# Performance work log

Measured on AMD Instinct MI355X. Metric: run time of the kernel, lower is better.

## Reference

```python
import jax, jax.numpy as jnp
import numpy as np

B, S, D, H = 2, 2048, 1024, 16
DEPTH = D // H


def setup_inputs() -> dict:
    key = jax.random.key(0)
    ks = jax.random.split(key, 10)
    std = 1.0 / np.sqrt(D)
    v = jax.random.normal(ks[0], (B, S, D), jnp.float32)
    q = jax.random.normal(ks[1], (B, S, D), jnp.float32)
    k = jax.random.normal(ks[2], (B, S, D), jnp.float32)
    # padding mask: 1.0 at masked (padded) key positions, 0.0 elsewhere
    mask = (jax.random.uniform(ks[3], (B, 1, 1, S)) < 0.1).astype(jnp.float32)
    Wq = jax.random.normal(ks[4], (D, D), jnp.float32) * std
    bq = jnp.zeros((D,), jnp.float32)
    Wv = jax.random.normal(ks[5], (D, D), jnp.float32) * std
    bv = jnp.zeros((D,), jnp.float32)
    Wo = jax.random.normal(ks[6], (D, D), jnp.float32) * std
    bo = jnp.zeros((D,), jnp.float32)
    return {"v": v, "q": q, "k": k, "mask": mask,
            "Wq": Wq, "bq": bq, "Wv": Wv, "bv": bv, "Wo": Wo, "bo": bo}


def _split_heads(x):
    # (B, S, D) -> (B, H, S, depth)
    return x.reshape(B, S, H, DEPTH).transpose(0, 2, 1, 3)


def reference(v, q, k, mask, Wq, bq, Wv, bv, Wo, bo):
    # NOTE: faithful to source, keys are projected with the QUERY weights
    # (mixedK = self.wQuery(k) in the original code).
    Q = _split_heads(q @ Wq + bq)
    K = _split_heads(k @ Wq + bq)
    V = _split_heads(v @ Wv + bv)
    scale = 1.0 / jnp.sqrt(jnp.asarray(DEPTH, jnp.float32))
    logits = jnp.einsum('bhqd,bhkd->bhqk', Q, K) * scale
    logits = logits + mask * (-1e9)
    attn = jax.nn.softmax(logits, axis=-1)
    out = jnp.einsum('bhqk,bhkd->bhqd', attn, V)
    out = out.transpose(0, 2, 1, 3).reshape(B, S, D)
    return out @ Wo + bo
```

## Files before the change

### kernel.cpp

```cpp
#include <hip/hip_runtime.h>
#include <cstddef>


namespace {

constexpr int Ss = 2048;
constexpr int Dd = 1024;
constexpr int Mm = 4096;
constexpr int NT = Ss / 64;
constexpr float QSCALE = 0.18033688f;
constexpr float NEG2 = -1.442695041e9f;

typedef unsigned short u16;
typedef __attribute__((ext_vector_type(8))) __bf16 bf16x8;
typedef __attribute__((ext_vector_type(4))) float f32x4;
typedef __attribute__((ext_vector_type(16))) float f32x16;
typedef __attribute__((ext_vector_type(4))) unsigned int u32x4;
typedef __attribute__((ext_vector_type(2))) unsigned int u32x2;

__device__ __forceinline__ u16 bfc(float f) {
  __bf16 h = (__bf16)f;
  return __builtin_bit_cast(u16, h);
}
__device__ __forceinline__ unsigned pack2(float lo, float hi) {
  return (unsigned)bfc(lo) | ((unsigned)bfc(hi) << 16);
}

__device__ __forceinline__ void gload_lds16(const void* g, void* l) {
  __builtin_amdgcn_global_load_lds(
      (__attribute__((address_space(1))) void*)g,
      (__attribute__((address_space(3))) void*)l, 16, 0, 0);
}

__device__ __forceinline__ f32x4 mfma16(bf16x8 a, bf16x8 b, f32x4 c) {
  return __builtin_amdgcn_mfma_f32_16x16x32_bf16(a, b, c, 0, 0, 0);
}
__device__ __forceinline__ f32x16 mfma32(bf16x8 a, bf16x8 b, f32x16 c) {
  return __builtin_amdgcn_mfma_f32_32x32x16_bf16(a, b, c, 0, 0, 0);
}
__device__ __forceinline__ float exp2_fast(float x) {
  return __builtin_amdgcn_exp2f(x);
}

__device__ __forceinline__ void pl32swap(unsigned& a, unsigned& b) {
#if __has_builtin(__builtin_amdgcn_permlane32_swap)
  u32x2 r = __builtin_amdgcn_permlane32_swap(a, b, false, false);
  a = r[0];
  b = r[1];
#else
  unsigned ax = (unsigned)__shfl_xor((int)a, 32);
  unsigned bx = (unsigned)__shfl_xor((int)b, 32);
  bool hi = (threadIdx.x & 63) >= 32;
  unsigned na = hi ? bx : a;
  unsigned nb = hi ? b : ax;
  a = na;
  b = nb;
#endif
}

__device__ __forceinline__ int swz(int row, int col) {
  return row * 64 + ((((col >> 3) ^ (row & 7)) << 3) | (col & 7));
}
__device__ __forceinline__ int src_col(int lane) {
  return ((lane & 7) ^ (lane >> 3)) * 8;
}

__global__ __launch_bounds__(256) void wt_transpose(const float* __restrict__ W0,
                                                    const float* __restrict__ W1,
                                                    const float* __restrict__ W2,
                                                    u16* __restrict__ wsbase) {
  const float* W = (blockIdx.z == 0) ? W0 : (blockIdx.z == 1) ? W1 : W2;
  u16* WT = wsbase + (size_t)blockIdx.z * (1024 * 1024);
  __shared__ float tile[32][33];
  const int tid = threadIdx.x;
  const int tx = tid & 31;
  const int ty = tid >> 5;
  const int n0 = blockIdx.x * 32;
  const int k0 = blockIdx.y * 32;
#pragma unroll
  for (int i = 0; i < 4; ++i)
    tile[ty + i * 8][tx] = W[(size_t)(k0 + ty + i * 8) * 1024 + n0 + tx];
  __syncthreads();
  const int r = tid >> 3;
  const int c4 = (tid & 7) * 4;
  ushort4 o4 = make_ushort4(bfc(tile[c4 + 0][r]), bfc(tile[c4 + 1][r]),
                            bfc(tile[c4 + 2][r]), bfc(tile[c4 + 3][r]));
  *(ushort4*)(&WT[(size_t)(n0 + r) * 1024 + k0 + c4]) = o4;
}

__global__ __launch_bounds__(256) void proj_qkv(
    const float* __restrict__ q, const float* __restrict__ k,
    const float* __restrict__ v, const u16* __restrict__ WqT,
    const u16* __restrict__ WvT, const float* __restrict__ bq,
    const float* __restrict__ bv, u16* __restrict__ Qp, u16* __restrict__ Kp,
    u16* __restrict__ VpT) {
  constexpr int K = 1024, N = 1024, M = 4096;
  __shared__ u16 As[128 * 64];
  __shared__ u16 Bs[128 * 64];
  const int lin = (int)blockIdx.x;
  const int xcd = lin & 7;
  const int j = lin >> 3;
  const int panel = xcd * 12 + (j >> 3);
  const int ntile = j & 7;
  const int z = panel >> 5;
  const int mtile = panel & 31;
  const int n0 = ntile * 128;
  const int m0 = mtile * 128;

  const float* A = (z == 0) ? q : (z == 1) ? k : v;
  const u16* Bt = (z == 2) ? WvT : WqT;
  const float* bias = (z == 2) ? bv : bq;
  const float cscale = (z == 0) ? QSCALE : 1.0f;

  const int tid = threadIdx.x;
  const int wid = tid >> 6;
  const int lane = tid & 63;
  const int g = lane >> 4;
  const int lr = lane & 15;
  const int wr = wid >> 1, wc = wid & 1;

  const f32x4 zero = {0.f, 0.f, 0.f, 0.f};
  f32x4 acc[4][4];
#pragma unroll
  for (int m = 0; m < 4; ++m)
#pragma unroll
    for (int n = 0; n < 4; ++n) acc[m][n] = zero;

  float4 areg[8];
  auto loadA = [&](int kt) {
#pragma unroll
    for (int i = 0; i < 8; ++i) {
      int e = i * 256 + tid;
      int row = e >> 4;
      int c4 = (e & 15) << 2;
      areg[i] = *(const float4*)(&A[(size_t)(m0 + row) * K + kt * 64 + c4]);
    }
  };
  auto writeA = [&]() {
#pragma unroll
    for (int i = 0; i < 8; ++i) {
      int e = i * 256 + tid;
      int row = e >> 4;
      int c4 = (e & 15) << 2;
      ushort4 o4 = make_ushort4(bfc(areg[i].x), bfc(areg[i].y), bfc(areg[i].z),
                                bfc(areg[i].w));
      *(ushort4*)(&As[swz(row, c4)]) = o4;
    }
  };

  loadA(0);
  for (int kt = 0; kt < 16; ++kt) {
    writeA();
#pragma unroll
    for (int jj = 0; jj < 4; ++jj) {
      int rb = (wid * 4 + jj) * 8;
      gload_lds16(&Bt[(size_t)(n0 + rb + (lane >> 3)) * K + kt * 64 + src_col(lane)],
                  &Bs[rb * 64]);
    }
    __syncthreads();
    if (kt + 1 < 16) loadA(kt + 1);
#pragma unroll
    for (int kk = 0; kk < 2; ++kk) {
      bf16x8 a[4], b[4];
#pragma unroll
      for (int m = 0; m < 4; ++m)
        a[m] = *(const bf16x8*)(&As[swz(wr * 64 + m * 16 + lr, kk * 32 + g * 8)]);
#pragma unroll
      for (int n = 0; n < 4; ++n)
        b[n] = *(const bf16x8*)(&Bs[swz(wc * 64 + n * 16 + lr, kk * 32 + g * 8)]);
#pragma unroll
      for (int m = 0; m < 4; ++m)
#pragma unroll
        for (int n = 0; n < 4; ++n) acc[m][n] = mfma16(a[m], b[n], acc[m][n]);
    }
    __syncthreads();
  }

#pragma unroll
  for (int n = 0; n < 4; ++n) {
    const int col = n0 + wc * 64 + n * 16 + lr;
    const float bv_ = bias[col];
#pragma unroll
    for (int m = 0; m < 4; ++m) {
      const int rowb = m0 + wr * 64 + m * 16 + g * 4;
      if (z == 2) {
        ushort4 o4 = make_ushort4(bfc(acc[m][n][0] + bv_), bfc(acc[m][n][1] + bv_),
                                  bfc(acc[m][n][2] + bv_), bfc(acc[m][n][3] + bv_));
        *(ushort4*)(&VpT[(size_t)col * M + rowb]) = o4;
      } else {
        u16* Cp = (z == 0) ? Qp : Kp;
#pragma unroll
        for (int r = 0; r < 4; ++r)
          Cp[(size_t)(rowb + r) * N + col] = bfc((acc[m][n][r] + bv_) * cscale);
      }
    }
  }
}

__global__ __launch_bounds__(256) void gemm_o(const u16* __restrict__ Ap,
                                              const u16* __restrict__ Bt,
                                              const float* __restrict__ bias,
                                              float* __restrict__ Cp) {
  constexpr int K = 1024, N = 1024;
  __shared__ u16 As[128 * 64];
  __shared__ u16 Bs[64 * 64];
  const int lin = (int)blockIdx.x;
  const int xcd = lin & 7;
  const int j = lin >> 3;
  const int mtile = xcd * 4 + (j >> 4);
  const int ntile = j & 15;
  const int n0 = ntile * 64;
  const int m0 = mtile * 128;

  const int tid = threadIdx.x;
  const int wid = tid >> 6;
  const int lane = tid & 63;
  const int g = lane >> 4;
  const int lr = lane & 15;

  const f32x4 zero = {0.f, 0.f, 0.f, 0.f};
  f32x4 acc[2][4];
#pragma unroll
  for (int m = 0; m < 2; ++m)
#pragma unroll
    for (int n = 0; n < 4; ++n) acc[m][n] = zero;

  for (int k0 = 0; k0 < K; k0 += 64) {
#pragma unroll
    for (int jj = 0; jj < 4; ++jj) {
      int rb = (wid * 4 + jj) * 8;
      gload_lds16(&Ap[(size_t)(m0 + rb + (lane >> 3)) * K + k0 + src_col(lane)],
                  &As[rb * 64]);
    }
#pragma unroll
    for (int jj = 0; jj < 2; ++jj) {
      int rb = (wid * 2 + jj) * 8;
      gload_lds16(&Bt[(size_t)(n0 + rb + (lane >> 3)) * K + k0 + src_col(lane)],
                  &Bs[rb * 64]);
    }
    __syncthreads();
#pragma unroll
    for (int kk = 0; kk < 2; ++kk) {
      bf16x8 a[2], b[4];
#pragma unroll
      for (int m = 0; m < 2; ++m)
        a[m] = *(const bf16x8*)(&As[swz(wid * 32 + m * 16 + lr, kk * 32 + g * 8)]);
#pragma unroll
      for (int n = 0; n < 4; ++n)
        b[n] = *(const bf16x8*)(&Bs[swz(n * 16 + lr, kk * 32 + g * 8)]);
#pragma unroll
      for (int m = 0; m < 2; ++m)
#pragma unroll
        for (int n = 0; n < 4; ++n) acc[m][n] = mfma16(a[m], b[n], acc[m][n]);
    }
    __syncthreads();
  }
#pragma unroll
  for (int n = 0; n < 4; ++n) {
    const int col = n0 + n * 16 + lr;
    const float bv_ = bias[col];
#pragma unroll
    for (int m = 0; m < 2; ++m) {
      const int rowb = m0 + wid * 32 + m * 16 + g * 4;
#pragma unroll
      for (int r = 0; r < 4; ++r)
        Cp[(size_t)(rowb + r) * N + col] = acc[m][n][r] + bv_;
    }
  }
}

__global__ __launch_bounds__(256) void attn32(const u16* __restrict__ Qp,
                                              const u16* __restrict__ Kp,
                                              const u16* __restrict__ VpT,
                                              const float* __restrict__ mask,
                                              u16* __restrict__ Op) {
  __shared__ u16 Ks[2][64 * 64];
  __shared__ u16 Vt[2][64 * 64];
  __shared__ float ms[2][64];
  __shared__ float redbuf[4][32];
  const int tid = threadIdx.x;
  const int wid = tid >> 6;
  const int lane = tid & 63;
  const int l31 = lane & 31;
  const int hi = lane >> 5;
  const int lin = (int)(blockIdx.x + (blockIdx.y << 4));
  const int wl = (lin & 7) * 64 + (lin >> 3);
  const int qt = wl & 15;
  const int bh = wl >> 4;
  const int b = bh >> 4;
  const int h = bh & 15;
  const int q0 = qt * 128;
  const size_t base = ((size_t)b * Ss) * Dd + (size_t)h * 64;
  const size_t vbase = (size_t)h * 64 * Mm + (size_t)b * Ss;
  const int qrow = q0 + wid * 32 + l31;

  bf16x8 qf[4];
#pragma unroll
  for (int ks = 0; ks < 4; ++ks)
    qf[ks] = *(const bf16x8*)(&Qp[base + (size_t)qrow * Dd + ks * 16 + hi * 8]);

  f32x16 oacc[2];
#pragma unroll
  for (int i = 0; i < 2; ++i)
#pragma unroll
    for (int r = 0; r < 16; ++r) oacc[i][r] = 0.f;
  float mrun = -1e30f, lrun = 0.f;

  auto stageKV = [&](int t, int buf) {
    const int key0 = t * 64;
#pragma unroll
    for (int jj = 0; jj < 2; ++jj) {
      int rb = (wid * 2 + jj) * 8;
      gload_lds16(&Kp[base + (size_t)(key0 + rb + (lane >> 3)) * Dd + src_col(lane)],
                  &Ks[buf][rb * 64]);
      gload_lds16(&VpT[vbase + (size_t)(rb + (lane >> 3)) * Mm + key0 + src_col(lane)],
                  &Vt[buf][rb * 64]);
    }
  };

  stageKV(0, 0);
  float msr = 0.f;
  if (tid < 64) ms[0][tid] = mask[(size_t)b * Ss + tid] * NEG2;
  __syncthreads();

  int cur = 0;
  for (int t = 0; t < NT; ++t) {
    const bool more = (t + 1) < NT;
    if (more) {
      stageKV(t + 1, cur ^ 1);
      if (tid < 64) msr = mask[(size_t)b * Ss + (t + 1) * 64 + tid];
    }
    f32x16 sacc[2];
#pragma unroll
    for (int i = 0; i < 2; ++i)
#pragma unroll
      for (int r = 0; r < 16; ++r) sacc[i][r] = 0.f;
    __builtin_amdgcn_s_setprio(1);
#pragma unroll
    for (int sub = 0; sub < 2; ++sub)
#pragma unroll
      for (int ks = 0; ks < 4; ++ks) {
        bf16x8 kf =
            *(const bf16x8*)(&Ks[cur][swz(sub * 32 + l31, ks * 16 + hi * 8)]);
        sacc[sub] = mfma32(kf, qf[ks], sacc[sub]);
      }
    __builtin_amdgcn_s_setprio(0);

    f32x4 mm[2][4];
#pragma unroll
    for (int sub = 0; sub < 2; ++sub)
#pragma unroll
      for (int a = 0; a < 4; ++a)
        mm[sub][a] = *(const f32x4*)(&ms[cur][sub * 32 + a * 8 + hi * 4]);
    float p[2][16];
#pragma unroll
    for (int sub = 0; sub < 2; ++sub)
#pragma unroll
      for (int r = 0; r < 16; ++r)
        p[sub][r] = sacc[sub][r] + mm[sub][r >> 2][r & 3];

    float mx[16];
#pragma unroll
    for (int r = 0; r < 16; ++r) mx[r] = fmaxf(p[0][r], p[1][r]);
#pragma unroll
    for (int s = 8; s >= 1; s >>= 1)
#pragma unroll
      for (int r = 0; r < s; ++r) mx[r] = fmaxf(mx[r], mx[r + s]);
    float rm = fmaxf(mx[0], __shfl_xor(mx[0], 32));

    if (__any(rm > mrun + 10.0f)) {
      const float mnew = fmaxf(mrun, rm);
      const float corr = exp2_fast(mrun - mnew);
      lrun *= corr;
      mrun = mnew;
      redbuf[wid][l31] = corr;
      f32x4 cv[4];
#pragma unroll
      for (int a = 0; a < 4; ++a)
        cv[a] = *(const f32x4*)(&redbuf[wid][a * 8 + hi * 4]);
#pragma unroll
      for (int d = 0; d < 2; ++d)
#pragma unroll
        for (int r = 0; r < 16; ++r) oacc[d][r] *= cv[r >> 2][r & 3];
    }
    float sm[16];
#pragma unroll
    for (int sub = 0; sub < 2; ++sub)
#pragma unroll
      for (int r = 0; r < 16; ++r) p[sub][r] = exp2_fast(p[sub][r] - mrun);
#pragma unroll
    for (int r = 0; r < 16; ++r) sm[r] = p[0][r] + p[1][r];
#pragma unroll
    for (int s = 8; s >= 1; s >>= 1)
#pragma unroll
      for (int r = 0; r < s; ++r) sm[r] += sm[r + s];
    lrun += sm[0] + __shfl_xor(sm[0], 32);

    bf16x8 pa[4];
#pragma unroll
    for (int sub = 0; sub < 2; ++sub)
#pragma unroll
      for (int half = 0; half < 2; ++half) {
        const int bse = half * 8;
        unsigned A0 = pack2(p[sub][bse + 0], p[sub][bse + 1]);
        unsigned A1 = pack2(p[sub][bse + 2], p[sub][bse + 3]);
        unsigned B0 = pack2(p[sub][bse + 4], p[sub][bse + 5]);
        unsigned B1 = pack2(p[sub][bse + 6], p[sub][bse + 7]);
        pl32swap(A0, B0);
        pl32swap(A1, B1);
        u32x4 w = {A0, A1, B0, B1};
        pa[sub * 2 + half] = __builtin_bit_cast(bf16x8, w);
      }

    __builtin_amdgcn_s_setprio(1);
#pragma unroll
    for (int dsub = 0; dsub < 2; ++dsub)
#pragma unroll
      for (int ks = 0; ks < 4; ++ks) {
        bf16x8 vf =
            *(const bf16x8*)(&Vt[cur][swz(dsub * 32 + l31, ks * 16 + hi * 8)]);
        oacc[dsub] = mfma32(pa[ks], vf, oacc[dsub]);
      }
    __builtin_amdgcn_s_setprio(0);

    if (more && tid < 64) ms[cur ^ 1][tid] = msr * NEG2;
    __syncthreads();
    cur ^= 1;
  }

  redbuf[wid][l31] = 1.0f / lrun;
  f32x4 cv[4];
#pragma unroll
  for (int a = 0; a < 4; ++a)
    cv[a] = *(const f32x4*)(&redbuf[wid][a * 8 + hi * 4]);
#pragma unroll
  for (int dsub = 0; dsub < 2; ++dsub) {
    const int col = h * 64 + dsub * 32 + l31;
#pragma unroll
    for (int r = 0; r < 16; ++r) {
      const int row = q0 + wid * 32 + (r & 3) + 8 * (r >> 2) + 4 * hi;
      Op[((size_t)b * Ss + row) * Dd + col] = bfc(oacc[dsub][r] * cv[r >> 2][r & 3]);
    }
  }
}

}

extern "C" void kernel_launch(void* const* d_in, const int* in_sizes, int n_in,
                              void* d_out, int out_size, void* d_ws, size_t ws_size,
                              hipStream_t stream) {
  (void)in_sizes; (void)n_in; (void)out_size; (void)ws_size;
  const float* v = (const float*)d_in[0];
  const float* q = (const float*)d_in[1];
  const float* k = (const float*)d_in[2];
  const float* mask = (const float*)d_in[3];
  const float* Wq = (const float*)d_in[4];
  const float* bq = (const float*)d_in[5];
  const float* Wv = (const float*)d_in[6];
  const float* bv = (const float*)d_in[7];
  const float* Wo = (const float*)d_in[8];
  const float* bo = (const float*)d_in[9];
  float* out = (float*)d_out;

  u16* ws = (u16*)d_ws;
  u16* WqT = ws;
  u16* WvT = WqT + 1024 * 1024;
  u16* WoT = WvT + 1024 * 1024;
  u16* Qp = WoT + 1024 * 1024;
  u16* Kp = Qp + 4096 * 1024;
  u16* VpT = Kp + 4096 * 1024;
  u16* AO = VpT + 4096 * 1024;

  wt_transpose<<<dim3(32, 32, 3), 256, 0, stream>>>(Wq, Wv, Wo, ws);
  proj_qkv<<<dim3(768), 256, 0, stream>>>(q, k, v, WqT, WvT, bq, bv, Qp, Kp, VpT);
  attn32<<<dim3(16, 32), 256, 0, stream>>>(Qp, Kp, VpT, mask, AO);
  gemm_o<<<dim3(512), 256, 0, stream>>>(AO, WoT, bo, out);
}
```

Baseline: 143.8 us.

## Pre-convert Q/K/V inputs to bf16 and load A tiles via direct global-to-LDS

Adds a separate kernel that converts the fp32 q, k, v inputs to bf16 in workspace, so the projection GEMM can stage its A operand with global_load_lds the same way it stages B. This drops the register-staged fp32 load, convert and LDS write path from the GEMM main loop. The cost is an extra launch plus an additional pass that reads the fp32 inputs and writes bf16 copies. The GEMM loop also loses its register prefetch of the next A tile. Separately, the attention kernel now seeds the score accumulators with the mask bias instead of adding it after the MFMA, which saves a register array and 32 adds per tile.

```diff
diff --git a/kernel.cpp b/kernel.cpp
--- a/kernel.cpp
+++ b/kernel.cpp
@@ -17,6 +17,7 @@
 typedef __attribute__((ext_vector_type(16))) float f32x16;
 typedef __attribute__((ext_vector_type(4))) unsigned int u32x4;
 typedef __attribute__((ext_vector_type(2))) unsigned int u32x2;
+typedef __attribute__((ext_vector_type(8))) unsigned short us8;
 
 __device__ __forceinline__ u16 bfc(float f) {
   __bf16 h = (__bf16)f;
@@ -88,9 +89,28 @@
   *(ushort4*)(&WT[(size_t)(n0 + r) * 1024 + k0 + c4]) = o4;
 }
 
+__global__ __launch_bounds__(256) void cvt_bf16(const float* __restrict__ q,
+                                                const float* __restrict__ k,
+                                                const float* __restrict__ v,
+                                                u16* __restrict__ qb,
+                                                u16* __restrict__ kb,
+                                                u16* __restrict__ vb) {
+  const int which = (int)(blockIdx.x >> 11);
+  const int blk = (int)(blockIdx.x & 2047);
+  const float* src = (which == 0) ? q : (which == 1) ? k : v;
+  u16* dst = (which == 0) ? qb : (which == 1) ? kb : vb;
+  const int base = (blk * 256 + (int)threadIdx.x) * 8;
+  const float4 a = *(const float4*)(src + base);
+  const float4 b = *(const float4*)(src + base + 4);
+  us8 o;
+  o[0] = bfc(a.x); o[1] = bfc(a.y); o[2] = bfc(a.z); o[3] = bfc(a.w);
+  o[4] = bfc(b.x); o[5] = bfc(b.y); o[6] = bfc(b.z); o[7] = bfc(b.w);
+  *(us8*)(dst + base) = o;
+}
+
 __global__ __launch_bounds__(256) void proj_qkv(
-    const float* __restrict__ q, const float* __restrict__ k,
-    const float* __restrict__ v, const u16* __restrict__ WqT,
+    const u16* __restrict__ qb, const u16* __restrict__ kb,
+    const u16* __restrict__ vb, const u16* __restrict__ WqT,
     const u16* __restrict__ WvT, const float* __restrict__ bq,
     const float* __restrict__ bv, u16* __restrict__ Qp, u16* __restrict__ Kp,
     u16* __restrict__ VpT) {
@@ -107,7 +127,7 @@
   const int n0 = ntile * 128;
   const int m0 = mtile * 128;
 
-  const float* A = (z == 0) ? q : (z == 1) ? k : v;
+  const u16* A = (z == 0) ? qb : (z == 1) ? kb : vb;
   const u16* Bt = (z == 2) ? WvT : WqT;
   const float* bias = (z == 2) ? bv : bq;
   const float cscale = (z == 0) ? QSCALE : 1.0f;
@@ -126,39 +146,16 @@
 #pragma unroll
     for (int n = 0; n < 4; ++n) acc[m][n] = zero;
 
-  float4 areg[8];
-  auto loadA = [&](int kt) {
-#pragma unroll
-    for (int i = 0; i < 8; ++i) {
-      int e = i * 256 + tid;
-      int row = e >> 4;
-      int c4 = (e & 15) << 2;
-      areg[i] = *(const float4*)(&A[(size_t)(m0 + row) * K + kt * 64 + c4]);
-    }
-  };
-  auto writeA = [&]() {
-#pragma unroll
-    for (int i = 0; i < 8; ++i) {
-      int e = i * 256 + tid;
-      int row = e >> 4;
-      int c4 = (e & 15) << 2;
-      ushort4 o4 = make_ushort4(bfc(areg[i].x), bfc(areg[i].y), bfc(areg[i].z),
-                                bfc(areg[i].w));
-      *(ushort4*)(&As[swz(row, c4)]) = o4;
-    }
-  };
-
-  loadA(0);
   for (int kt = 0; kt < 16; ++kt) {
-    writeA();
 #pragma unroll
     for (int jj = 0; jj < 4; ++jj) {
       int rb = (wid * 4 + jj) * 8;
+      gload_lds16(&A[(size_t)(m0 + rb + (lane >> 3)) * K + kt * 64 + src_col(lane)],
+                  &As[rb * 64]);
       gload_lds16(&Bt[(size_t)(n0 + rb + (lane >> 3)) * K + kt * 64 + src_col(lane)],
                   &Bs[rb * 64]);
     }
     __syncthreads();
-    if (kt + 1 < 16) loadA(kt + 1);
 #pragma unroll
     for (int kk = 0; kk < 2; ++kk) {
       bf16x8 a[4], b[4];
@@ -332,9 +329,13 @@
     }
     f32x16 sacc[2];
 #pragma unroll
-    for (int i = 0; i < 2; ++i)
-#pragma unroll
-      for (int r = 0; r < 16; ++r) sacc[i][r] = 0.f;
+    for (int sub = 0; sub < 2; ++sub)
+#pragma unroll
+      for (int a = 0; a < 4; ++a) {
+        const f32x4 mv = *(const f32x4*)(&ms[cur][sub * 32 + a * 8 + hi * 4]);
+#pragma unroll
+        for (int jj = 0; jj < 4; ++jj) sacc[sub][a * 4 + jj] = mv[jj];
+      }
     __builtin_amdgcn_s_setprio(1);
 #pragma unroll
     for (int sub = 0; sub < 2; ++sub)
@@ -346,22 +347,9 @@
       }
     __builtin_amdgcn_s_setprio(0);
 
-    f32x4 mm[2][4];
-#pragma unroll
-    for (int sub = 0; sub < 2; ++sub)
-#pragma unroll
-      for (int a = 0; a < 4; ++a)
-        mm[sub][a] = *(const f32x4*)(&ms[cur][sub * 32 + a * 8 + hi * 4]);
-    float p[2][16];
-#pragma unroll
-    for (int sub = 0; sub < 2; ++sub)
-#pragma unroll
-      for (int r = 0; r < 16; ++r)
-        p[sub][r] = sacc[sub][r] + mm[sub][r >> 2][r & 3];
-
     float mx[16];
 #pragma unroll
-    for (int r = 0; r < 16; ++r) mx[r] = fmaxf(p[0][r], p[1][r]);
+    for (int r = 0; r < 16; ++r) mx[r] = fmaxf(sacc[0][r], sacc[1][r]);
 #pragma unroll
     for (int s = 8; s >= 1; s >>= 1)
 #pragma unroll
@@ -387,9 +375,9 @@
 #pragma unroll
     for (int sub = 0; sub < 2; ++sub)
 #pragma unroll
-      for (int r = 0; r < 16; ++r) p[sub][r] = exp2_fast(p[sub][r] - mrun);
-#pragma unroll
-    for (int r = 0; r < 16; ++r) sm[r] = p[0][r] + p[1][r];
+      for (int r = 0; r < 16; ++r) sacc[sub][r] = exp2_fast(sacc[sub][r] - mrun);
+#pragma unroll
+    for (int r = 0; r < 16; ++r) sm[r] = sacc[0][r] + sacc[1][r];
 #pragma unroll
     for (int s = 8; s >= 1; s >>= 1)
 #pragma unroll
@@ -402,10 +390,10 @@
 #pragma unroll
       for (int half = 0; half < 2; ++half) {
         const int bse = half * 8;
-        unsigned A0 = pack2(p[sub][bse + 0], p[sub][bse + 1]);
-        unsigned A1 = pack2(p[sub][bse + 2], p[sub][bse + 3]);
-        unsigned B0 = pack2(p[sub][bse + 4], p[sub][bse + 5]);
-        unsigned B1 = pack2(p[sub][bse + 6], p[sub][bse + 7]);
+        unsigned A0 = pack2(sacc[sub][bse + 0], sacc[sub][bse + 1]);
+        unsigned A1 = pack2(sacc[sub][bse + 2], sacc[sub][bse + 3]);
+        unsigned B0 = pack2(sacc[sub][bse + 4], sacc[sub][bse + 5]);
+        unsigned B1 = pack2(sacc[sub][bse + 6], sacc[sub][bse + 7]);
         pl32swap(A0, B0);
         pl32swap(A1, B1);
         u32x4 w = {A0, A1, B0, B1};
@@ -462,17 +450,22 @@
   const float* bo = (const float*)d_in[9];
   float* out = (float*)d_out;
 
+  constexpr size_t MEG = 1024 * 1024;
   u16* ws = (u16*)d_ws;
   u16* WqT = ws;
-  u16* WvT = WqT + 1024 * 1024;
-  u16* WoT = WvT + 1024 * 1024;
-  u16* Qp = WoT + 1024 * 1024;
-  u16* Kp = Qp + 4096 * 1024;
-  u16* VpT = Kp + 4096 * 1024;
-  u16* AO = VpT + 4096 * 1024;
+  u16* WvT = ws + 1 * MEG;
+  u16* WoT = ws + 2 * MEG;
+  u16* qb  = ws + 3 * MEG;
+  u16* kb  = ws + 7 * MEG;
+  u16* vb  = ws + 11 * MEG;
+  u16* Qp  = ws + 15 * MEG;
+  u16* Kp  = ws + 19 * MEG;
+  u16* VpT = ws + 23 * MEG;
+  u16* AO  = qb;
 
   wt_transpose<<<dim3(32, 32, 3), 256, 0, stream>>>(Wq, Wv, Wo, ws);
-  proj_qkv<<<dim3(768), 256, 0, stream>>>(q, k, v, WqT, WvT, bq, bv, Qp, Kp, VpT);
+  cvt_bf16<<<dim3(6144), 256, 0, stream>>>(q, k, v, qb, kb, vb);
+  proj_qkv<<<dim3(768), 256, 0, stream>>>(qb, kb, vb, WqT, WvT, bq, bv, Qp, Kp, VpT);
   attn32<<<dim3(16, 32), 256, 0, stream>>>(Qp, Kp, VpT, mask, AO);
   gemm_o<<<dim3(512), 256, 0, stream>>>(AO, WoT, bo, out);
 }
```

Result: no change. 143.9 us (+0.1%).
